# Kernel tuning notes

Hardware: AMD Instinct MI355X
Metric: run time of the kernel (lower is better)

Reference implementation:

```python
import jax, jax.numpy as jnp
import numpy as np

N = 4096
TAU = 0.2          # args.tau relaxation temperature
EPS = 1e-10        # numerical guard for logit of clamped probs


def setup_inputs() -> dict:
    key = jax.random.key(0)
    k1, k2, k3 = jax.random.split(key, 3)
    r = jax.random.uniform(k1, (N, N))
    ori_adj = jnp.where(r < 0.005, -1.0, jnp.where(r < 0.01, 1.0, 0.0)).astype(jnp.float32)
    # nn.init.uniform_(change_links_prob, 0.0, 0.001)
    change_links_prob = jax.random.uniform(k2, (N, N), minval=0.0, maxval=0.001, dtype=jnp.float32)
    # uniform noise for the RelaxedBernoulli logistic reparameterization
    u = jax.random.uniform(k3, (N, N), minval=1e-6, maxval=1.0 - 1e-6, dtype=jnp.float32)
    return {"ori_adj": ori_adj, "change_links_prob": change_links_prob, "u": u}


def reference(ori_adj, change_links_prob, u):
    # --- get_modified_adj: RelaxedBernoulliStraightThrough(tau, clamp(p,0,1)).rsample() ---
    p = jnp.clip(change_links_prob, EPS, 1.0 - EPS)      # torch.clamp(p, 0, 1) + logit guard
    logits = jnp.log(p) - jnp.log1p(-p)
    noise = jnp.log(u) - jnp.log1p(-u)                   # logistic noise
    soft = jax.nn.sigmoid((logits + noise) / TAU)        # relaxed sample
    hard = jnp.round(soft)                               # quantized sample
    change_prob = soft + jax.lax.stop_gradient(hard - soft)  # straight-through
    mod_adj = ori_adj + change_prob * (-2.0 * ori_adj)   # ori_adj * (1 - 2*b)

    # --- balance_degree_directed(mod_adj) ---
    # torch.diag(matrix) returns the diagonal VECTOR, broadcast-subtracted per row (faithful).
    A = mod_adj + mod_adj.T - jnp.diag(mod_adj)
    A_abs = jnp.abs(A)
    tr3 = jnp.einsum('ij,jk,ki->', A, A, A)              # trace(A @ A @ A)
    tr3_abs = jnp.einsum('ij,jk,ki->', A_abs, A_abs, A_abs)
    balance = 0.5 * (1.0 + tr3 / tr3_abs)
    return mod_adj, balance
```

## Files before the change

kernel.cpp:

```cpp
#include <hip/hip_runtime.h>
#include <hip/hip_bf16.h>
#include <cstdint>
#include <cstddef>

#define N 4096
#define NN ((size_t)N * (size_t)N)

typedef int int4v __attribute__((ext_vector_type(4)));

__device__ inline void async16(const void* g, void* lds) {
    __builtin_amdgcn_global_load_lds(
        (const __attribute__((address_space(1))) void*)g,
        (__attribute__((address_space(3))) void*)lds, 16, 0, 0);
}

__global__ void mod_kernel(const float* __restrict__ ori,
                           const float* __restrict__ clp,
                           const float* __restrict__ u,
                           float* __restrict__ out) {
    size_t i = (size_t)blockIdx.x * blockDim.x + threadIdx.x;
    if (i >= NN) return;
    float p = clp[i];
    p = fminf(fmaxf(p, 1e-10f), 1.0f - 1e-10f);
    float logits = logf(p) - log1pf(-p);
    float uu = u[i];
    float noise = logf(uu) - log1pf(-uu);
    float y = (logits + noise) / 0.2f;
    float soft = 1.0f / (1.0f + expf(-y));
    float hard = rintf(soft);
    float o = ori[i];
    out[i] = o + hard * (-2.0f * o);
}

__global__ void diag_kernel(const float* __restrict__ mod,
                            float* __restrict__ diag,
                            double* __restrict__ accs) {
    int j = blockIdx.x * blockDim.x + threadIdx.x;
    if (j < N) diag[j] = mod[(size_t)j * N + j];
    if (blockIdx.x == 0 && threadIdx.x < 2) accs[threadIdx.x] = 0.0;
}

__global__ void build_A8(const float* __restrict__ mod,
                         const float* __restrict__ diag,
                         signed char* __restrict__ A,
                         signed char* __restrict__ AT,
                         signed char* __restrict__ Aa,
                         signed char* __restrict__ ATa) {
    __shared__ float tji[32][33];
    __shared__ signed char cv[32][36];
    const int bi = blockIdx.x * 32;
    const int bj = blockIdx.y * 32;
    const int tx = threadIdx.x;
    const int ty = threadIdx.y;
    {
        const float4 v = *(const float4*)&mod[(size_t)(bj + ty) * N + bi + tx * 4];
        tji[ty][tx * 4 + 0] = v.x; tji[ty][tx * 4 + 1] = v.y;
        tji[ty][tx * 4 + 2] = v.z; tji[ty][tx * 4 + 3] = v.w;
    }
    __syncthreads();
    const float4 mv = *(const float4*)&mod[(size_t)(bi + ty) * N + bj + tx * 4];
    float m4[4] = {mv.x, mv.y, mv.z, mv.w};
    int pkA = 0, pkAa = 0;
    #pragma unroll
    for (int k = 0; k < 4; ++k) {
        int jl = tx * 4 + k;
        float a = m4[k] + tji[jl][ty] - diag[bj + jl];
        int ai = (int)a;
        cv[ty][jl] = (signed char)ai;
        int au = ai < 0 ? -ai : ai;
        pkA  |= (ai & 255) << (8 * k);
        pkAa |= (au & 255) << (8 * k);
    }
    *(int*)&A [(size_t)(bi + ty) * N + bj + tx * 4] = pkA;
    *(int*)&Aa[(size_t)(bi + ty) * N + bj + tx * 4] = pkAa;
    __syncthreads();
    int pkT = 0, pkTa = 0;
    #pragma unroll
    for (int k = 0; k < 4; ++k) {
        int il = tx * 4 + k;
        int v = cv[il][ty];
        int va = v < 0 ? -v : v;
        pkT  |= (v  & 255) << (8 * k);
        pkTa |= (va & 255) << (8 * k);
    }
    *(int*)&AT [(size_t)(bj + ty) * N + bi + tx * 4] = pkT;
    *(int*)&ATa[(size_t)(bj + ty) * N + bi + tx * 4] = pkTa;
}

__global__ __launch_bounds__(256) void gemm_trace_i8(const signed char* __restrict__ Ag,
                                                     const signed char* __restrict__ ATg,
                                                     const signed char* __restrict__ Aag,
                                                     const signed char* __restrict__ ATag,
                                                     double* __restrict__ accs) {
    __shared__ int4v As4[512];
    __shared__ int4v Bs4[512];
    __shared__ int red[4];
    const int z = blockIdx.z;
    const signed char* Asrc = z ? Aag  : Ag;
    const signed char* Bsrc = z ? ATag : ATg;
    const int i0 = blockIdx.y * 128;
    const int k0 = blockIdx.x * 128;
    const int t = threadIdx.x;
    const int lane = t & 63;
    const int wave = t >> 6;
    const int quad = lane >> 4;
    const int col  = lane & 15;
    const int wr = (wave >> 1) * 64;
    const int wc = (wave & 1) * 64;
    signed char* Asc = (signed char*)As4;
    signed char* Bsc = (signed char*)Bs4;

    const int c0 = wave * 64 + lane;
    const int c1 = c0 + 256;
    const int r0 = c0 >> 2, r1 = c1 >> 2;
    const int cc0 = (((c0 & 3) ^ ((r0 >> 1) & 3)) << 4);
    const int cc1 = (((c1 & 3) ^ ((r1 >> 1) & 3)) << 4);
    const int ldsb0 = (wave * 64) << 4;
    const int ldsb1 = (256 + wave * 64) << 4;
    const signed char* gA0 = Asrc + (size_t)(i0 + r0) * N + cc0;
    const signed char* gA1 = Asrc + (size_t)(i0 + r1) * N + cc1;
    const signed char* gB0 = Bsrc + (size_t)(k0 + r0) * N + cc0;
    const signed char* gB1 = Bsrc + (size_t)(k0 + r1) * N + cc1;

    int4v acc[4][4];
    #pragma unroll
    for (int a = 0; a < 4; ++a)
        #pragma unroll
        for (int b = 0; b < 4; ++b)
            acc[a][b] = (int4v){0, 0, 0, 0};

    const int fsw = ((quad ^ ((col >> 1) & 3)) << 4);

    for (int kb = 0; kb < N; kb += 64) {
        __syncthreads();
        async16(gA0 + kb, Asc + ldsb0);
        async16(gA1 + kb, Asc + ldsb1);
        async16(gB0 + kb, Bsc + ldsb0);
        async16(gB1 + kb, Bsc + ldsb1);
        __syncthreads();
        int4v af[4], bf[4];
        #pragma unroll
        for (int tr = 0; tr < 4; ++tr)
            af[tr] = *(const int4v*)(Asc + ((wr + tr * 16 + col) << 6) + fsw);
        #pragma unroll
        for (int tc = 0; tc < 4; ++tc)
            bf[tc] = *(const int4v*)(Bsc + ((wc + tc * 16 + col) << 6) + fsw);
        #pragma unroll
        for (int tr = 0; tr < 4; ++tr)
            #pragma unroll
            for (int tc = 0; tc < 4; ++tc)
                acc[tr][tc] = __builtin_amdgcn_mfma_i32_16x16x64_i8(af[tr], bf[tc], acc[tr][tc], 0, 0, 0);
    }

    int part = 0;
    #pragma unroll
    for (int tr = 0; tr < 4; ++tr) {
        #pragma unroll
        for (int tc = 0; tc < 4; ++tc) {
            const int ib = i0 + wr + tr * 16 + quad * 4;
            const int kk = k0 + wc + tc * 16 + col;
            #pragma unroll
            for (int r = 0; r < 4; ++r)
                part += acc[tr][tc][r] * (int)Bsrc[(size_t)(ib + r) * N + kk];
        }
    }
    #pragma unroll
    for (int off = 32; off > 0; off >>= 1)
        part += __shfl_down(part, off, 64);
    if (lane == 0) red[wave] = part;
    __syncthreads();
    if (t == 0) {
        int tot = red[0] + red[1] + red[2] + red[3];
        atomicAdd(&accs[z], (double)tot);
    }
}

__global__ void finalize_kernel(const double* __restrict__ accs, float* __restrict__ out) {
    out[NN] = (float)(0.5 * (1.0 + accs[0] / accs[1]));
}

extern "C" void kernel_launch(void* const* d_in, const int* in_sizes, int n_in,
                              void* d_out, int out_size, void* d_ws, size_t ws_size,
                              hipStream_t stream) {
    const float* ori = (const float*)d_in[0];
    const float* clp = (const float*)d_in[1];
    const float* u   = (const float*)d_in[2];
    float* out = (float*)d_out;
    char* ws = (char*)d_ws;
    signed char* A8   = (signed char*)ws;
    signed char* AT8  = (signed char*)(ws + NN);
    signed char* Aa8  = (signed char*)(ws + 2 * NN);
    signed char* ATa8 = (signed char*)(ws + 3 * NN);
    float*       diag = (float*)(ws + 4 * NN);
    double*      accs = (double*)(ws + 4 * NN + 4096 * 4);

    mod_kernel<<<dim3((unsigned)(NN / 256)), 256, 0, stream>>>(ori, clp, u, out);
    diag_kernel<<<dim3(16), 256, 0, stream>>>(out, diag, accs);
    build_A8<<<dim3(N / 32, N / 32), dim3(8, 32), 0, stream>>>(out, diag, A8, AT8, Aa8, ATa8);
    gemm_trace_i8<<<dim3(N / 128, N / 128, 2), 256, 0, stream>>>(A8, AT8, Aa8, ATa8, accs);
    finalize_kernel<<<1, 1, 0, stream>>>(accs, out);
}
```

Before: 426.3 us.

## Multi-stage pipelined 256x256 int8 MFMA GEMM with vectorized elementwise kernel

Result: no change. 428.0 us (+0.4%).

```diff
diff --git a/kernel.cpp b/kernel.cpp
--- a/kernel.cpp
+++ b/kernel.cpp
@@ -6,7 +6,8 @@
 #define N 4096
 #define NN ((size_t)N * (size_t)N)
 
-typedef int int4v __attribute__((ext_vector_type(4)));
+typedef int   int4v   __attribute__((ext_vector_type(4)));
+typedef float float4v __attribute__((ext_vector_type(4)));
 
 __device__ inline void async16(const void* g, void* lds) {
     __builtin_amdgcn_global_load_lds(
@@ -18,18 +19,24 @@
                            const float* __restrict__ clp,
                            const float* __restrict__ u,
                            float* __restrict__ out) {
-    size_t i = (size_t)blockIdx.x * blockDim.x + threadIdx.x;
-    if (i >= NN) return;
-    float p = clp[i];
-    p = fminf(fmaxf(p, 1e-10f), 1.0f - 1e-10f);
-    float logits = logf(p) - log1pf(-p);
-    float uu = u[i];
-    float noise = logf(uu) - log1pf(-uu);
-    float y = (logits + noise) / 0.2f;
-    float soft = 1.0f / (1.0f + expf(-y));
-    float hard = rintf(soft);
-    float o = ori[i];
-    out[i] = o + hard * (-2.0f * o);
+    size_t i = ((size_t)blockIdx.x * blockDim.x + threadIdx.x) * 4;
+    const float4v p4 = *(const float4v*)(clp + i);
+    const float4v u4 = *(const float4v*)(u + i);
+    const float4v o4 = *(const float4v*)(ori + i);
+    float4v r;
+    #pragma unroll
+    for (int c = 0; c < 4; ++c) {
+        float p = fminf(fmaxf(p4[c], 1e-10f), 1.0f - 1e-10f);
+        float logits = logf(p) - log1pf(-p);
+        float uu = u4[c];
+        float noise = logf(uu) - log1pf(-uu);
+        float y = (logits + noise) / 0.2f;
+        float soft = 1.0f / (1.0f + expf(-y));
+        float hard = rintf(soft);
+        float o = o4[c];
+        r[c] = o + hard * (-2.0f * o);
+    }
+    *(float4v*)(out + i) = r;
 }
 
 __global__ void diag_kernel(const float* __restrict__ mod,
@@ -87,81 +94,128 @@
     *(int*)&ATa[(size_t)(bj + ty) * N + bi + tx * 4] = pkTa;
 }
 
-__global__ __launch_bounds__(256) void gemm_trace_i8(const signed char* __restrict__ Ag,
-                                                     const signed char* __restrict__ ATg,
-                                                     const signed char* __restrict__ Aag,
-                                                     const signed char* __restrict__ ATag,
-                                                     double* __restrict__ accs) {
-    __shared__ int4v As4[512];
-    __shared__ int4v Bs4[512];
-    __shared__ int red[4];
+#define BK 64
+#define NT (N / BK)
+#define BUFSZ 32768
+
+__global__ __launch_bounds__(512, 2) void gemm_trace_i8(
+        const signed char* __restrict__ Ag,
+        const signed char* __restrict__ ATg,
+        const signed char* __restrict__ Aag,
+        const signed char* __restrict__ ATag,
+        double* __restrict__ accs) {
+    __shared__ __align__(16) signed char lds[4 * BUFSZ];
+    __shared__ int red[8];
     const int z = blockIdx.z;
     const signed char* Asrc = z ? Aag  : Ag;
     const signed char* Bsrc = z ? ATag : ATg;
-    const int i0 = blockIdx.y * 128;
-    const int k0 = blockIdx.x * 128;
+    const int i0 = blockIdx.y * 256;
+    const int k0 = blockIdx.x * 256;
     const int t = threadIdx.x;
     const int lane = t & 63;
     const int wave = t >> 6;
+    const int wm = wave >> 2;
+    const int wn = wave & 3;
     const int quad = lane >> 4;
     const int col  = lane & 15;
-    const int wr = (wave >> 1) * 64;
-    const int wc = (wave & 1) * 64;
-    signed char* Asc = (signed char*)As4;
-    signed char* Bsc = (signed char*)Bs4;
-
-    const int c0 = wave * 64 + lane;
-    const int c1 = c0 + 256;
-    const int r0 = c0 >> 2, r1 = c1 >> 2;
-    const int cc0 = (((c0 & 3) ^ ((r0 >> 1) & 3)) << 4);
-    const int cc1 = (((c1 & 3) ^ ((r1 >> 1) & 3)) << 4);
-    const int ldsb0 = (wave * 64) << 4;
-    const int ldsb1 = (256 + wave * 64) << 4;
-    const signed char* gA0 = Asrc + (size_t)(i0 + r0) * N + cc0;
-    const signed char* gA1 = Asrc + (size_t)(i0 + r1) * N + cc1;
-    const signed char* gB0 = Bsrc + (size_t)(k0 + r0) * N + cc0;
-    const signed char* gB1 = Bsrc + (size_t)(k0 + r1) * N + cc1;
-
-    int4v acc[4][4];
-    #pragma unroll
-    for (int a = 0; a < 4; ++a)
+
+    const int c1 = t;
+    const int r1 = c1 >> 2;
+    const int r2 = r1 + 128;
+    const int s1 = (((c1 & 3) ^ ((r1 >> 1) & 3)) << 4);
+    const int s2 = (((c1 & 3) ^ ((r2 >> 1) & 3)) << 4);
+    const signed char* gA1 = Asrc + (size_t)(i0 + r1) * N + s1;
+    const signed char* gA2 = Asrc + (size_t)(i0 + r2) * N + s2;
+    const signed char* gB1 = Bsrc + (size_t)(k0 + r1) * N + s1;
+    const signed char* gB2 = Bsrc + (size_t)(k0 + r2) * N + s2;
+    const int ldsA1 = (wave * 64) * 16;
+    const int ldsA2 = 8192  + (wave * 64) * 16;
+    const int ldsB1 = 16384 + (wave * 64) * 16;
+    const int ldsB2 = 24576 + (wave * 64) * 16;
+    const int fsw = ((quad ^ ((col >> 1) & 3)) << 4);
+
+    int4v acc[8][4];
+    #pragma unroll
+    for (int a = 0; a < 8; ++a)
         #pragma unroll
         for (int b = 0; b < 4; ++b)
             acc[a][b] = (int4v){0, 0, 0, 0};
 
-    const int fsw = ((quad ^ ((col >> 1) & 3)) << 4);
-
-    for (int kb = 0; kb < N; kb += 64) {
-        __syncthreads();
-        async16(gA0 + kb, Asc + ldsb0);
-        async16(gA1 + kb, Asc + ldsb1);
-        async16(gB0 + kb, Bsc + ldsb0);
-        async16(gB1 + kb, Bsc + ldsb1);
-        __syncthreads();
-        int4v af[4], bf[4];
-        #pragma unroll
-        for (int tr = 0; tr < 4; ++tr)
-            af[tr] = *(const int4v*)(Asc + ((wr + tr * 16 + col) << 6) + fsw);
+    for (int p = 0; p < 3; ++p) {
+        const int pb = p * BUFSZ;
+        const size_t go = (size_t)p * BK;
+        async16(gA1 + go, lds + pb + ldsA1);
+        async16(gA2 + go, lds + pb + ldsA2);
+        async16(gB1 + go, lds + pb + ldsB1);
+        async16(gB2 + go, lds + pb + ldsB2);
+    }
+    asm volatile("s_waitcnt vmcnt(8)" ::: "memory");
+    __builtin_amdgcn_s_barrier();
+
+    int4v bf[4];
+    for (int j = 0; j < NT; ++j) {
+        const int buf = (j & 3) * BUFSZ;
+        const signed char* Ab = lds + buf;
+        const signed char* Bb = lds + buf + 16384;
+        const int pre = j + 3;
+        const size_t go = (size_t)pre * BK;
+        const int pb = (pre & 3) * BUFSZ;
+        int4v af[4];
+        #pragma unroll
+        for (int tr = 0; tr < 4; ++tr)
+            af[tr] = *(const int4v*)(Ab + ((wm * 128 + tr * 16 + col) << 6) + fsw);
         #pragma unroll
         for (int tc = 0; tc < 4; ++tc)
-            bf[tc] = *(const int4v*)(Bsc + ((wc + tc * 16 + col) << 6) + fsw);
+            bf[tc] = *(const int4v*)(Bb + ((wn * 64 + tc * 16 + col) << 6) + fsw);
+        if (pre < NT) {
+            async16(gA1 + go, lds + pb + ldsA1);
+            async16(gA2 + go, lds + pb + ldsA2);
+        }
+        __builtin_amdgcn_s_barrier();
+        asm volatile("s_waitcnt lgkmcnt(0)" ::: "memory");
+        __builtin_amdgcn_sched_barrier(0);
+        __builtin_amdgcn_s_setprio(1);
         #pragma unroll
         for (int tr = 0; tr < 4; ++tr)
             #pragma unroll
             for (int tc = 0; tc < 4; ++tc)
                 acc[tr][tc] = __builtin_amdgcn_mfma_i32_16x16x64_i8(af[tr], bf[tc], acc[tr][tc], 0, 0, 0);
+        __builtin_amdgcn_s_setprio(0);
+        __builtin_amdgcn_s_barrier();
+        #pragma unroll
+        for (int tr = 0; tr < 4; ++tr)
+            af[tr] = *(const int4v*)(Ab + ((wm * 128 + 64 + tr * 16 + col) << 6) + fsw);
+        if (pre < NT) {
+            async16(gB1 + go, lds + pb + ldsB1);
+            async16(gB2 + go, lds + pb + ldsB2);
+        }
+        __builtin_amdgcn_s_barrier();
+        asm volatile("s_waitcnt lgkmcnt(0)" ::: "memory");
+        __builtin_amdgcn_sched_barrier(0);
+        __builtin_amdgcn_s_setprio(1);
+        #pragma unroll
+        for (int tr = 0; tr < 4; ++tr)
+            #pragma unroll
+            for (int tc = 0; tc < 4; ++tc)
+                acc[4 + tr][tc] = __builtin_amdgcn_mfma_i32_16x16x64_i8(af[tr], bf[tc], acc[4 + tr][tc], 0, 0, 0);
+        __builtin_amdgcn_s_setprio(0);
+        if (j < NT - 3)       { asm volatile("s_waitcnt vmcnt(8)" ::: "memory"); }
+        else if (j == NT - 3) { asm volatile("s_waitcnt vmcnt(4)" ::: "memory"); }
+        else if (j == NT - 2) { asm volatile("s_waitcnt vmcnt(0)" ::: "memory"); }
+        __builtin_amdgcn_s_barrier();
     }
 
     int part = 0;
     #pragma unroll
-    for (int tr = 0; tr < 4; ++tr) {
+    for (int mr = 0; mr < 8; ++mr) {
+        const int ib = i0 + wm * 128 + mr * 16 + quad * 4;
         #pragma unroll
         for (int tc = 0; tc < 4; ++tc) {
-            const int ib = i0 + wr + tr * 16 + quad * 4;
-            const int kk = k0 + wc + tc * 16 + col;
+            const int kk = k0 + wn * 64 + tc * 16 + col;
+            const int mv = *(const int*)&Asrc[(size_t)kk * N + ib];
             #pragma unroll
             for (int r = 0; r < 4; ++r)
-                part += acc[tr][tc][r] * (int)Bsrc[(size_t)(ib + r) * N + kk];
+                part += acc[mr][tc][r] * (int)(signed char)(mv >> (8 * r));
         }
     }
     #pragma unroll
@@ -170,7 +224,9 @@
     if (lane == 0) red[wave] = part;
     __syncthreads();
     if (t == 0) {
-        int tot = red[0] + red[1] + red[2] + red[3];
+        int tot = 0;
+        #pragma unroll
+        for (int w = 0; w < 8; ++w) tot += red[w];
         atomicAdd(&accs[z], (double)tot);
     }
 }
@@ -194,9 +250,9 @@
     float*       diag = (float*)(ws + 4 * NN);
     double*      accs = (double*)(ws + 4 * NN + 4096 * 4);
 
-    mod_kernel<<<dim3((unsigned)(NN / 256)), 256, 0, stream>>>(ori, clp, u, out);
+    mod_kernel<<<dim3((unsigned)(NN / 1024)), 256, 0, stream>>>(ori, clp, u, out);
     diag_kernel<<<dim3(16), 256, 0, stream>>>(out, diag, accs);
     build_A8<<<dim3(N / 32, N / 32), dim3(8, 32), 0, stream>>>(out, diag, A8, AT8, Aa8, ATa8);
-    gemm_trace_i8<<<dim3(N / 128, N / 128, 2), 256, 0, stream>>>(A8, AT8, Aa8, ATa8, accs);
+    gemm_trace_i8<<<dim3(N / 256, N / 256, 2), 512, 0, stream>>>(A8, AT8, Aa8, ATa8, accs);
     finalize_kernel<<<1, 1, 0, stream>>>(accs, out);
 }
```
